# Kernel optimization log

Measured on AMD Instinct MI355X. Metric: run time of the kernel, lower is better.

Reference implementation:

```python
import jax, jax.numpy as jnp
import numpy as np

N_NODES = 100000
N_EDGES = 3200000
N_FEAT = 16
N_LAYERS = 4


def setup_inputs() -> dict:
    key = jax.random.key(0)
    k1, k2, k3, k4 = jax.random.split(key, 4)
    h_0 = jax.random.normal(k1, (N_NODES, N_FEAT), dtype=jnp.float32)
    edge_index = jax.random.randint(k2, (2, N_EDGES), 0, N_NODES, dtype=jnp.int64)
    weight_tensor = jax.random.normal(k3, (N_EDGES,), dtype=jnp.float32)
    # per-layer learned per-edge weights, init normal(std=1/sqrt(E)) as in torch
    layer_weights = jax.random.normal(k4, (N_LAYERS, N_EDGES), dtype=jnp.float32) / np.sqrt(N_EDGES)
    return {"h_0": h_0, "edge_index": edge_index, "weight_tensor": weight_tensor,
            "layer_weights": layer_weights}


def _layer(h, src, dst, edge_scale):
    # gather x_j = h[src]  [E, F], scale by per-edge scalar, scatter-add to dst
    msg = edge_scale[:, None] * h[src]
    return jax.ops.segment_sum(msg, dst, num_segments=N_NODES)


def reference(h_0, edge_index, weight_tensor, layer_weights):
    # PyG default flow source_to_target: x_j = x[edge_index[0]], aggregate at edge_index[1]
    src = edge_index[0]
    dst = edge_index[1]
    h = h_0
    for k in range(N_LAYERS - 1):
        h = _layer(h, src, dst, weight_tensor * layer_weights[k])
        h = h + h_0
    h = _layer(h, src, dst, weight_tensor * layer_weights[N_LAYERS - 1])
    return jax.nn.sigmoid(2.0 * h)
```

## Files before the change

### kernel.cpp

```cpp
#include <hip/hip_runtime.h>
#include <hip/hip_fp16.h>

#define NNODES   100000
#define NFEAT    16
#define NEDGES   3200000
#define EH       1600000
#define NB       250
#define NODES_PB 400
#define NCHH     500
#define NCH2     1000
#define CHK      3200
#define CAP      7168
#define N8       (NNODES * 8)

__global__ __launch_bounds__(256) void hist_chunk(
    const int* __restrict__ dst, int* __restrict__ cnt )
{
    __shared__ int h[NB];
    int c = blockIdx.x;
    for (int i = threadIdx.x; i < NB; i += 256) h[i] = 0;
    __syncthreads();
    int base = c * CHK;
    for (int i = threadIdx.x; i < CHK; i += 256) {
        int d = dst[base + i];
        atomicAdd(&h[d / NODES_PB], 1);
    }
    __syncthreads();
    for (int i = threadIdx.x; i < NB; i += 256) cnt[c * NB + i] = h[i];
}

__global__ __launch_bounds__(512) void scan_chunks(
    int* __restrict__ cnt, int* __restrict__ tot )
{
    __shared__ int x[512];
    int half = blockIdx.x / NB;
    int b    = blockIdx.x % NB;
    int t = threadIdx.x;
    int v = (t < NCHH) ? cnt[(half * NCHH + t) * NB + b] : 0;
    x[t] = v;
    __syncthreads();
    for (int off = 1; off < 512; off <<= 1) {
        int y = (t >= off) ? x[t - off] : 0;
        __syncthreads();
        x[t] += y;
        __syncthreads();
    }
    if (t < NCHH) cnt[(half * NCHH + t) * NB + b] = x[t] - v;
    if (t == NCHH - 1) tot[half * NB + b] = x[t];
}

__global__ __launch_bounds__(256) void scan_tot(
    const int* __restrict__ tot, int* __restrict__ bb)
{
    __shared__ int x[256];
    int half = blockIdx.x;
    const int* tt = tot + half * NB;
    int* bbh = bb + half * (NB + 1);
    int t = threadIdx.x;
    int v = (t < NB) ? tt[t] : 0;
    x[t] = v;
    __syncthreads();
    for (int off = 1; off < 256; off <<= 1) {
        int y = (t >= off) ? x[t - off] : 0;
        __syncthreads();
        x[t] += y;
        __syncthreads();
    }
    if (t < NB) bbh[t] = x[t] - v;
    if (t == NB - 1) bbh[NB] = x[t];
}

__global__ __launch_bounds__(256) void scatter_bins(
    const int*   __restrict__ src,
    const int*   __restrict__ dst,
    const float* __restrict__ wt,
    const float* __restrict__ lw,
    const int*   __restrict__ cnt,
    const int*   __restrict__ bb,
    unsigned int* __restrict__ binsE )
{
    __shared__ int cur[NB];
    int c = blockIdx.x;
    int half = c / NCHH;
    const int* bbh = bb + half * (NB + 1);
    unsigned int* bE = binsE + (size_t)half * 3 * EH;
    for (int i = threadIdx.x; i < NB; i += 256)
        cur[i] = bbh[i] + cnt[c * NB + i];
    __syncthreads();
    int base = c * CHK;
    for (int i = threadIdx.x; i < CHK; i += 256) {
        int e = base + i;
        int d = dst[e];
        int b  = d / NODES_PB;
        int dl = d - b * NODES_PB;
        float w = wt[e];
        __half2 w01 = __floats2half2_rn(w * lw[e],              w * lw[NEDGES + e]);
        __half2 w23 = __floats2half2_rn(w * lw[2 * NEDGES + e], w * lw[3 * NEDGES + e]);
        int slot = atomicAdd(&cur[b], 1);
        unsigned int* p = bE + 3u * (unsigned int)slot;
        p[0] = (unsigned int)src[e] | ((unsigned int)dl << 17);
        p[1] = *(const unsigned int*)&w01;
        p[2] = *(const unsigned int*)&w23;
    }
}

__global__ __launch_bounds__(512) void bucket_csr(
    const int*          __restrict__ bb,
    const unsigned int* __restrict__ binsE,
    unsigned int*       __restrict__ csrA   ,
    unsigned short*     __restrict__ wbase  ,
    int*                __restrict__ offs   )
{
    __shared__ unsigned int   regA[CAP];
    __shared__ unsigned int   regC[CAP];
    __shared__ unsigned short pi[CAP];
    __shared__ int hist[NODES_PB];
    __shared__ int cur[NODES_PB];
    __shared__ int sc[512];
    int g = blockIdx.x, t = threadIdx.x;
    int half = g / NB;
    int b    = g % NB;
    const int* bbh = bb + half * (NB + 1);
    const unsigned int* bE = binsE + (size_t)half * 3 * EH;
    unsigned int*   cA = csrA + (size_t)half * EH;
    unsigned short* w0 = wbase + (size_t)(half * 4 + 0) * EH;
    unsigned short* w1 = wbase + (size_t)(half * 4 + 1) * EH;
    unsigned short* w2 = wbase + (size_t)(half * 4 + 2) * EH;
    unsigned short* w3 = wbase + (size_t)(half * 4 + 3) * EH;
    int* offsh = offs + half * (NNODES + 1);

    int e0 = bbh[b];
    int cnt = bbh[b + 1] - e0;
    if (cnt > CAP) cnt = CAP;

    for (int i = t; i < NODES_PB; i += 512) hist[i] = 0;
    __syncthreads();
    for (int i = t; i < cnt; i += 512) {
        unsigned int a = bE[3u * (unsigned int)(e0 + i)];
        regA[i] = a;
        atomicAdd(&hist[a >> 17], 1);
    }
    __syncthreads();
    int v = (t < NODES_PB) ? hist[t] : 0;
    sc[t] = v;
    __syncthreads();
    for (int off = 1; off < 512; off <<= 1) {
        int y = (t >= off) ? sc[t - off] : 0;
        __syncthreads();
        sc[t] += y;
        __syncthreads();
    }
    if (t < NODES_PB) {
        int excl = sc[t] - v;
        cur[t] = excl;
        offsh[b * NODES_PB + t] = e0 + excl;
    }
    if (b == 0 && t == 0) offsh[NNODES] = EH;
    __syncthreads();
    unsigned short* inv = (unsigned short*)regC;
    for (int i = t; i < cnt; i += 512) {
        unsigned int a = regA[i];
        int slot = atomicAdd(&cur[a >> 17], 1);
        pi[i]  = (unsigned short)slot;
        inv[slot] = (unsigned short)i;
    }
    __syncthreads();
    for (int s = t; s < cnt; s += 512) {
        cA[e0 + s] = regA[inv[s]] & 0x1FFFFu;
    }
    __syncthreads();
    unsigned short* wA0 = (unsigned short*)regA;
    unsigned short* wA1 = wA0 + CAP;
    unsigned short* wC2 = (unsigned short*)regC;
    unsigned short* wC3 = wC2 + CAP;
    for (int i = t; i < cnt; i += 512) {
        unsigned int u01 = bE[3u * (unsigned int)(e0 + i) + 1];
        unsigned int u23 = bE[3u * (unsigned int)(e0 + i) + 2];
        int s = pi[i];
        wA0[s] = (unsigned short)(u01 & 0xFFFFu);
        wA1[s] = (unsigned short)(u01 >> 16);
        wC2[s] = (unsigned short)(u23 & 0xFFFFu);
        wC3[s] = (unsigned short)(u23 >> 16);
    }
    __syncthreads();
    for (int s = t; s < cnt; s += 512) {
        w0[e0 + s] = wA0[s];
        w1[e0 + s] = wA1[s];
        w2[e0 + s] = wC2[s];
        w3[e0 + s] = wC3[s];
    }
}

__global__ __launch_bounds__(256) void conv16(
    const float2* __restrict__ in, __half2* __restrict__ out, int n2)
{
    int i = blockIdx.x * 256 + threadIdx.x;
    if (i < n2) {
        float2 v = in[i];
        out[i] = __floats2half2_rn(v.x, v.y);
    }
}

template<bool SIG>
__global__ __launch_bounds__(256) void pullr(
    const int*            __restrict__ offs1,
    const int*            __restrict__ offs2,
    const unsigned int*   __restrict__ csrA1,
    const unsigned int*   __restrict__ csrA2,
    const unsigned short* __restrict__ wk1,
    const unsigned short* __restrict__ wk2,
    const __half2*        __restrict__ h16,
    const float2*         __restrict__ h0,
    void*                 __restrict__ hout)
{
    int t = blockIdx.x * 256 + threadIdx.x;
    int n = t >> 5;
    if (n >= NNODES) return;
    int grp = (t >> 3) & 3;
    int f2  = t & 7;

    int j01 = offs1[n], e1 = offs1[n + 1];
    int j02 = offs2[n], e2 = offs2[n + 1];
    int m1 = (j01 + e1) >> 1;
    int m2 = (j02 + e2) >> 1;

    const unsigned int*   A;
    const unsigned short* W;
    int js, je;
    if (grp < 2) {
        A = csrA1; W = wk1;
        js = (grp == 0) ? j01 : m1;
        je = (grp == 0) ? m1  : e1;
    } else {
        A = csrA2; W = wk2;
        js = (grp == 2) ? j02 : m2;
        je = (grp == 2) ? m2  : e2;
    }

    float ax = 0.f, ay = 0.f;
    int j = js;
    for (; j + 3 < je; j += 4) {
        unsigned int s0 = A[j],     s1 = A[j + 1];
        unsigned int s2 = A[j + 2], s3 = A[j + 3];
        float w0 = __half2float(__ushort_as_half(W[j]));
        float w1 = __half2float(__ushort_as_half(W[j + 1]));
        float w2 = __half2float(__ushort_as_half(W[j + 2]));
        float w3 = __half2float(__ushort_as_half(W[j + 3]));
        float2 v0 = __half22float2(h16[s0 * 8 + f2]);
        float2 v1 = __half22float2(h16[s1 * 8 + f2]);
        float2 v2 = __half22float2(h16[s2 * 8 + f2]);
        float2 v3 = __half22float2(h16[s3 * 8 + f2]);
        ax = fmaf(w0, v0.x, ax); ay = fmaf(w0, v0.y, ay);
        ax = fmaf(w1, v1.x, ax); ay = fmaf(w1, v1.y, ay);
        ax = fmaf(w2, v2.x, ax); ay = fmaf(w2, v2.y, ay);
        ax = fmaf(w3, v3.x, ax); ay = fmaf(w3, v3.y, ay);
    }
    for (; j < je; ++j) {
        unsigned int s = A[j];
        float w = __half2float(__ushort_as_half(W[j]));
        float2 v = __half22float2(h16[s * 8 + f2]);
        ax = fmaf(w, v.x, ax); ay = fmaf(w, v.y, ay);
    }

    ax += __shfl_xor(ax, 8);  ay += __shfl_xor(ay, 8);
    ax += __shfl_xor(ax, 16); ay += __shfl_xor(ay, 16);

    if (grp == 0) {
        int o = n * 8 + f2;
        if (SIG) {
            float2 r;
            r.x = 1.f / (1.f + expf(-2.f * ax));
            r.y = 1.f / (1.f + expf(-2.f * ay));
            ((float2*)hout)[o] = r;
        } else {
            float2 b = h0[o];
            ((__half2*)hout)[o] = __floats2half2_rn(ax + b.x, ay + b.y);
        }
    }
}

__global__ __launch_bounds__(256) void scatter_layer(
    const int* __restrict__ src, const int* __restrict__ dst,
    const float* __restrict__ wt, const float* __restrict__ lw,
    const float* __restrict__ h, float* __restrict__ acc)
{
    long t = (long)blockIdx.x * blockDim.x + threadIdx.x;
    int e = (int)(t >> 4);
    if (e >= NEDGES) return;
    int f = (int)(t & 15);
    float w = wt[e] * lw[e];
    atomicAdd(&acc[dst[e] * NFEAT + f], w * h[src[e] * NFEAT + f]);
}
__global__ __launch_bounds__(256) void sigmoid_inplace(float* __restrict__ out, int n)
{
    int i = blockIdx.x * blockDim.x + threadIdx.x;
    if (i < n) out[i] = 1.f / (1.f + expf(-2.f * out[i]));
}

extern "C" void kernel_launch(void* const* d_in, const int* in_sizes, int n_in,
                              void* d_out, int out_size, void* d_ws, size_t ws_size,
                              hipStream_t stream)
{
    const float* h0 = (const float*)d_in[0];
    const int*   ei = (const int*)d_in[1];
    const float* wt = (const float*)d_in[2];
    const float* lw = (const float*)d_in[3];

    const int* src = ei;
    const int* dst = ei + NEDGES;

    const size_t off_cnt  = 0;
    const size_t off_tot  = 1000064;
    const size_t off_bb   = 1002112;
    const size_t off_offs = 1004160;
    const size_t off_csrA = 1804288;
    const size_t off_w    = off_csrA + (size_t)2 * EH * 4;
    const size_t off_bins = off_w + (size_t)8 * EH * 2;
    const size_t need     = off_bins + (size_t)2 * 3 * EH * 4;

    if (ws_size < need) {
        const size_t hbytes = (size_t)NNODES * NFEAT * sizeof(float);
        float* hw = (float*)d_ws;
        float* ho = (float*)d_out;
        dim3 blk(256), grd(((long)NEDGES * 16 + 255) / 256);
        hipMemcpyAsync(hw, h0, hbytes, hipMemcpyDeviceToDevice, stream);
        scatter_layer<<<grd, blk, 0, stream>>>(src, dst, wt, lw + 0L * NEDGES, h0, hw);
        hipMemcpyAsync(ho, h0, hbytes, hipMemcpyDeviceToDevice, stream);
        scatter_layer<<<grd, blk, 0, stream>>>(src, dst, wt, lw + 1L * NEDGES, hw, ho);
        hipMemcpyAsync(hw, h0, hbytes, hipMemcpyDeviceToDevice, stream);
        scatter_layer<<<grd, blk, 0, stream>>>(src, dst, wt, lw + 2L * NEDGES, ho, hw);
        hipMemsetAsync(ho, 0, hbytes, stream);
        scatter_layer<<<grd, blk, 0, stream>>>(src, dst, wt, lw + 3L * NEDGES, hw, ho);
        int n = NNODES * NFEAT;
        sigmoid_inplace<<<(n + 255) / 256, 256, 0, stream>>>(ho, n);
        return;
    }

    char* ws = (char*)d_ws;
    int*            cnt   = (int*)(ws + off_cnt);
    int*            tot   = (int*)(ws + off_tot);
    int*            bb    = (int*)(ws + off_bb);
    int*            offs  = (int*)(ws + off_offs);
    int*            offs1 = offs;
    int*            offs2 = offs + (NNODES + 1);
    unsigned int*   csrA  = (unsigned int*)(ws + off_csrA);
    unsigned int*   csrA1 = csrA;
    unsigned int*   csrA2 = csrA + EH;
    unsigned short* wbase = (unsigned short*)(ws + off_w);
    unsigned short* w0_1 = wbase + 0L * EH; unsigned short* w1_1 = wbase + 1L * EH;
    unsigned short* w2_1 = wbase + 2L * EH; unsigned short* w3_1 = wbase + 3L * EH;
    unsigned short* w0_2 = wbase + 4L * EH; unsigned short* w1_2 = wbase + 5L * EH;
    unsigned short* w2_2 = wbase + 6L * EH; unsigned short* w3_2 = wbase + 7L * EH;
    unsigned int*   binsE = (unsigned int*)(ws + off_bins);
    const size_t HB = (size_t)NNODES * NFEAT * 2;
    __half2* hb0  = (__half2*)(ws + off_bins);
    __half2* hbA  = (__half2*)(ws + off_bins + HB);
    __half2* hbB  = (__half2*)d_out;
    float*   hout = (float*)d_out;

    hist_chunk  <<<NCH2,   256, 0, stream>>>(dst, cnt);
    scan_chunks <<<2 * NB, 512, 0, stream>>>(cnt, tot);
    scan_tot    <<<2,      256, 0, stream>>>(tot, bb);
    scatter_bins<<<NCH2,   256, 0, stream>>>(src, dst, wt, lw, cnt, bb, binsE);
    bucket_csr  <<<2 * NB, 512, 0, stream>>>(bb, binsE, csrA, wbase, offs);

    conv16<<<(N8 + 255) / 256, 256, 0, stream>>>((const float2*)h0, hb0, N8);

    dim3 blk(256), grdP((NNODES * 32) / 256);
    const float2* h0f2 = (const float2*)h0;
    pullr<false><<<grdP, blk, 0, stream>>>(offs1, offs2, csrA1, csrA2, w0_1, w0_2, hb0, h0f2, hbA);
    pullr<false><<<grdP, blk, 0, stream>>>(offs1, offs2, csrA1, csrA2, w1_1, w1_2, hbA, h0f2, hbB);
    pullr<false><<<grdP, blk, 0, stream>>>(offs1, offs2, csrA1, csrA2, w2_1, w2_2, hbB, h0f2, hbA);
    pullr<true ><<<grdP, blk, 0, stream>>>(offs1, offs2, csrA1, csrA2, w3_1, w3_2, hbA, h0f2, hout);
}
```

Before: 227.1 us.

## Stage scatter_bins output in shared memory for contiguous per-bin global writes

scatter_bins now computes a local per-chunk histogram from the cnt/tot exclusive-prefix arrays, scans it in shared memory, and places each edge's packed record into a shared buffer sorted by bin. A second pass then writes the records to global memory in slot order, so consecutive threads write consecutive addresses within each bin rather than scattered 12-byte records. The block size grows to 512, and shared memory use rises to roughly 45KB per block, which may reduce occupancy.

```diff
diff --git a/kernel.cpp b/kernel.cpp
--- a/kernel.cpp
+++ b/kernel.cpp
@@ -70,25 +70,57 @@
     if (t == NB - 1) bbh[NB] = x[t];
 }
 
-__global__ __launch_bounds__(256) void scatter_bins(
+__global__ __launch_bounds__(512) void scatter_bins(
     const int*   __restrict__ src,
     const int*   __restrict__ dst,
     const float* __restrict__ wt,
     const float* __restrict__ lw,
     const int*   __restrict__ cnt,
+    const int*   __restrict__ tot,
     const int*   __restrict__ bb,
     unsigned int* __restrict__ binsE )
 {
-    __shared__ int cur[NB];
+    __shared__ unsigned int   sE[CHK * 3];
+    __shared__ unsigned short sB[CHK];
+    __shared__ int lhist[NB];
+    __shared__ int loff[NB];
+    __shared__ int lcur[NB];
+    __shared__ int gmb[NB];
+    __shared__ int x[512];
+
     int c = blockIdx.x;
+    int t = threadIdx.x;
     int half = c / NCHH;
+    int cc   = c % NCHH;
     const int* bbh = bb + half * (NB + 1);
     unsigned int* bE = binsE + (size_t)half * 3 * EH;
-    for (int i = threadIdx.x; i < NB; i += 256)
-        cur[i] = bbh[i] + cnt[c * NB + i];
-    __syncthreads();
+
+    for (int i = t; i < NB; i += 512) {
+        int cur0 = cnt[c * NB + i];
+        int nxt  = (cc == NCHH - 1) ? tot[half * NB + i] : cnt[(c + 1) * NB + i];
+        lhist[i] = nxt - cur0;
+        gmb[i]   = bbh[i] + cur0;
+    }
+    __syncthreads();
+    int v = (t < NB) ? lhist[t] : 0;
+    x[t] = v;
+    __syncthreads();
+    for (int off = 1; off < 512; off <<= 1) {
+        int y = (t >= off) ? x[t - off] : 0;
+        __syncthreads();
+        x[t] += y;
+        __syncthreads();
+    }
+    if (t < NB) {
+        int excl = x[t] - v;
+        loff[t] = excl;
+        lcur[t] = excl;
+        gmb[t] -= excl;
+    }
+    __syncthreads();
+
     int base = c * CHK;
-    for (int i = threadIdx.x; i < CHK; i += 256) {
+    for (int i = t; i < CHK; i += 512) {
         int e = base + i;
         int d = dst[e];
         int b  = d / NODES_PB;
@@ -96,11 +128,21 @@
         float w = wt[e];
         __half2 w01 = __floats2half2_rn(w * lw[e],              w * lw[NEDGES + e]);
         __half2 w23 = __floats2half2_rn(w * lw[2 * NEDGES + e], w * lw[3 * NEDGES + e]);
-        int slot = atomicAdd(&cur[b], 1);
-        unsigned int* p = bE + 3u * (unsigned int)slot;
-        p[0] = (unsigned int)src[e] | ((unsigned int)dl << 17);
-        p[1] = *(const unsigned int*)&w01;
-        p[2] = *(const unsigned int*)&w23;
+        int slot = atomicAdd(&lcur[b], 1);
+        sE[3 * slot + 0] = (unsigned int)src[e] | ((unsigned int)dl << 17);
+        sE[3 * slot + 1] = *(const unsigned int*)&w01;
+        sE[3 * slot + 2] = *(const unsigned int*)&w23;
+        sB[slot] = (unsigned short)b;
+    }
+    __syncthreads();
+
+    for (int s = t; s < CHK; s += 512) {
+        int b = sB[s];
+        unsigned int g = (unsigned int)(gmb[b] + s);
+        unsigned int* p = bE + 3u * g;
+        p[0] = sE[3 * s + 0];
+        p[1] = sE[3 * s + 1];
+        p[2] = sE[3 * s + 2];
     }
 }
 
@@ -361,7 +403,7 @@
     hist_chunk  <<<NCH2,   256, 0, stream>>>(dst, cnt);
     scan_chunks <<<2 * NB, 512, 0, stream>>>(cnt, tot);
     scan_tot    <<<2,      256, 0, stream>>>(tot, bb);
-    scatter_bins<<<NCH2,   256, 0, stream>>>(src, dst, wt, lw, cnt, bb, binsE);
+    scatter_bins<<<NCH2,   512, 0, stream>>>(src, dst, wt, lw, cnt, tot, bb, binsE);
     bucket_csr  <<<2 * NB, 512, 0, stream>>>(bb, binsE, csrA, wbase, offs);
 
     conv16<<<(N8 + 255) / 256, 256, 0, stream>>>((const float2*)h0, hb0, N8);
```

After: 207.8 us. 8.5% less time.
